# Optimization experiments

Hardware: AMD Instinct MI355X
Metric: run time of the kernel (lower is better)

## Reference

```python
import jax, jax.numpy as jnp
import numpy as np

H = 4096
W = 4096
C = 3
OUT = 1024
MAX_MIP = 8  # matches init max_mip_level; mip chain is levels 0..MAX_MIP


def setup_inputs() -> dict:
    key = jax.random.key(0)
    k1, k2, k3 = jax.random.split(key, 3)
    data = jax.random.uniform(k1, (1, H, W, C), dtype=jnp.float32)
    texc = jax.random.uniform(k2, (1, OUT, OUT, 2), dtype=jnp.float32)
    # small UV derivatives -> per-pixel texel footprint of a few texels, so the
    # LOD spans several mip levels (exercises cross-level paged gathers)
    texc_deriv = jax.random.normal(k3, (1, OUT, OUT, 4), dtype=jnp.float32) * 2e-3
    return {"data": data, "texc": texc, "texc_deriv": texc_deriv}


def _avg_pool2(x):
    # 2x2 box-filter mipmap reduction, matching virtual_texture_mipmap_fwd
    b, h, w, c = x.shape
    return x.reshape(b, h // 2, 2, w // 2, 2, c).mean(axis=(2, 4))


def _bilinear_wrap(tex, texc):
    # tex: [1,h,w,c]; texc: [1,Ho,Wo,2] in [0,1); boundary_mode='wrap'
    h, w = tex.shape[1], tex.shape[2]
    x = texc[..., 0] * w - 0.5
    y = texc[..., 1] * h - 0.5
    x0f = jnp.floor(x)
    y0f = jnp.floor(y)
    fx = (x - x0f)[..., None]
    fy = (y - y0f)[..., None]
    x0 = x0f.astype(jnp.int32) % w
    y0 = y0f.astype(jnp.int32) % h
    x1 = (x0 + 1) % w
    y1 = (y0 + 1) % h
    t = tex[0]  # [h,w,c]
    top = t[y0, x0] * (1.0 - fx) + t[y0, x1] * fx
    bot = t[y1, x0] * (1.0 - fx) + t[y1, x1] * fx
    return top * (1.0 - fy) + bot * fy  # [1,Ho,Wo,c]


def _forward(data, texc, texc_deriv):
    # LOD from screen-space UV derivatives (nvdiffrast linear-mipmap-linear)
    dudx = texc_deriv[..., 0] * W
    dvdx = texc_deriv[..., 1] * H
    dudy = texc_deriv[..., 2] * W
    dvdy = texc_deriv[..., 3] * H
    rho2 = jnp.maximum(dudx * dudx + dvdx * dvdx, dudy * dudy + dvdy * dvdy)
    lod = 0.5 * jnp.log2(jnp.maximum(rho2, 1e-20))
    lod = jnp.clip(lod, 0.0, float(MAX_MIP))  # [1,Ho,Wo]

    # build mip pyramid (gradients flow back to base texture, matching
    # virtual_texture_mipmap_bwd accumulation)
    mips = [data]
    for _ in range(MAX_MIP):
        mips.append(_avg_pool2(mips[-1]))

    # trilinear: per-level weight w_l = clip(1 - |lod - l|, 0, 1)
    out = jnp.zeros(texc.shape[:-1] + (C,), dtype=data.dtype)
    for lvl in range(MAX_MIP + 1):
        w_l = jnp.clip(1.0 - jnp.abs(lod - float(lvl)), 0.0, 1.0)[..., None]
        out = out + w_l * _bilinear_wrap(mips[lvl], texc)
    return out


def reference(data, texc, texc_deriv):
    return _forward(data, texc, texc_deriv)
```

## Files before the change

### kernel.cpp

```cpp
#include <hip/hip_runtime.h>
#include <hip/hip_bf16.h>


#define OUT_N (1024 * 1024)

__device__ __forceinline__ unsigned mip_off_b(int lvl) {
    return (67108864u - (67108864u >> (2 * lvl - 2))) / 3u;
}

__device__ __forceinline__ unsigned pack10(float r, float g, float b) {
    unsigned ur = __float2uint_rn(r * 1023.0f);
    unsigned ug = __float2uint_rn(g * 1023.0f);
    unsigned ub = __float2uint_rn(b * 1023.0f);
    return ur | (ug << 10) | (ub << 20);
}

__device__ __forceinline__ void dec_acc(unsigned q, float w, float& r, float& g, float& b) {
    const float s = 1.0f / 1023.0f;
    r = fmaf((float)(q & 1023u) * s, w, r);
    g = fmaf((float)((q >> 10) & 1023u) * s, w, g);
    b = fmaf((float)((q >> 20) & 1023u) * s, w, b);
}

__device__ __forceinline__ float4 dec4(unsigned q) {
    const float s = 1.0f / 1023.0f;
    return float4{(float)(q & 1023u) * s, (float)((q >> 10) & 1023u) * s,
                  (float)((q >> 20) & 1023u) * s, 0.0f};
}

__device__ __forceinline__ float4 avg4(float4 a, float4 b, float4 c, float4 d) {
    return float4{(a.x + b.x + c.x + d.x) * 0.25f,
                  (a.y + b.y + c.y + d.y) * 0.25f,
                  (a.z + b.z + c.z + d.z) * 0.25f, 0.0f};
}

__device__ __forceinline__ void store_quad(char* p, float4 t00, float4 t01,
                                           float4 t10, float4 t11) {
    *(uint4*)p = make_uint4(pack10(t00.x, t00.y, t00.z), pack10(t01.x, t01.y, t01.z),
                            pack10(t10.x, t10.y, t10.z), pack10(t11.x, t11.y, t11.z));
}

__global__ __launch_bounds__(256) void mip_fused(const float* __restrict__ data,
                                                 char* __restrict__ wsb) {
    __shared__ float4 s1[32][33];
    __shared__ float4 s2[16][17];
    __shared__ float4 s3[8][9];
    __shared__ float4 s4[4][5];

    const int t = threadIdx.x;
    const int bx = blockIdx.x & 63;
    const int by = blockIdx.x >> 6;

    {
        int qx = t & 15, qy = t >> 4;
        int r0 = (by << 6) + (qy << 2);
        int c0 = (bx << 6) + (qx << 2);
        const float* p = data + ((size_t)r0 * 4096 + c0) * 3;
        float4 t00 = {0, 0, 0, 0}, t01 = {0, 0, 0, 0};
        float4 t10 = {0, 0, 0, 0}, t11 = {0, 0, 0, 0};
#pragma unroll
        for (int i = 0; i < 4; ++i) {
            const float4* rp = (const float4*)(p + (size_t)i * 4096 * 3);
            float4 A = rp[0], B = rp[1], C = rp[2];
            float ex = A.x + A.w, ey = A.y + B.x, ez = A.z + B.y;
            float fx_ = B.z + C.y, fy_ = B.w + C.z, fz_ = C.x + C.w;
            if (i < 2) {
                t00.x += ex; t00.y += ey; t00.z += ez;
                t01.x += fx_; t01.y += fy_; t01.z += fz_;
            } else {
                t10.x += ex; t10.y += ey; t10.z += ez;
                t11.x += fx_; t11.y += fy_; t11.z += fz_;
            }
        }
        t00.x *= 0.25f; t00.y *= 0.25f; t00.z *= 0.25f;
        t01.x *= 0.25f; t01.y *= 0.25f; t01.z *= 0.25f;
        t10.x *= 0.25f; t10.y *= 0.25f; t10.z *= 0.25f;
        t11.x *= 0.25f; t11.y *= 0.25f; t11.z *= 0.25f;
        s1[2 * qy][2 * qx] = t00;     s1[2 * qy][2 * qx + 1] = t01;
        s1[2 * qy + 1][2 * qx] = t10; s1[2 * qy + 1][2 * qx + 1] = t11;
        unsigned gq = (((by << 4) + qy) << 10) + (bx << 4) + qx;
        store_quad(wsb + ((size_t)gq << 4), t00, t01, t10, t11);
    }
    __syncthreads();

    if (t < 64) {
        int qx = t & 7, qy = t >> 3;
        int sy = qy << 2, sx = qx << 2;
        float4 t00 = avg4(s1[sy][sx], s1[sy][sx + 1], s1[sy + 1][sx], s1[sy + 1][sx + 1]);
        float4 t01 = avg4(s1[sy][sx + 2], s1[sy][sx + 3], s1[sy + 1][sx + 2], s1[sy + 1][sx + 3]);
        float4 t10 = avg4(s1[sy + 2][sx], s1[sy + 2][sx + 1], s1[sy + 3][sx], s1[sy + 3][sx + 1]);
        float4 t11 = avg4(s1[sy + 2][sx + 2], s1[sy + 2][sx + 3], s1[sy + 3][sx + 2], s1[sy + 3][sx + 3]);
        s2[2 * qy][2 * qx] = t00;     s2[2 * qy][2 * qx + 1] = t01;
        s2[2 * qy + 1][2 * qx] = t10; s2[2 * qy + 1][2 * qx + 1] = t11;
        unsigned gq = ((by << 3) + qy) * 512 + (bx << 3) + qx;
        store_quad(wsb + 16777216u + ((size_t)gq << 4), t00, t01, t10, t11);
    }
    __syncthreads();

    if (t < 16) {
        int qx = t & 3, qy = t >> 2;
        int sy = qy << 2, sx = qx << 2;
        float4 t00 = avg4(s2[sy][sx], s2[sy][sx + 1], s2[sy + 1][sx], s2[sy + 1][sx + 1]);
        float4 t01 = avg4(s2[sy][sx + 2], s2[sy][sx + 3], s2[sy + 1][sx + 2], s2[sy + 1][sx + 3]);
        float4 t10 = avg4(s2[sy + 2][sx], s2[sy + 2][sx + 1], s2[sy + 3][sx], s2[sy + 3][sx + 1]);
        float4 t11 = avg4(s2[sy + 2][sx + 2], s2[sy + 2][sx + 3], s2[sy + 3][sx + 2], s2[sy + 3][sx + 3]);
        s3[2 * qy][2 * qx] = t00;     s3[2 * qy][2 * qx + 1] = t01;
        s3[2 * qy + 1][2 * qx] = t10; s3[2 * qy + 1][2 * qx + 1] = t11;
        unsigned gq = ((by << 2) + qy) * 256 + (bx << 2) + qx;
        store_quad(wsb + 20971520u + ((size_t)gq << 4), t00, t01, t10, t11);
    }
    __syncthreads();

    if (t < 4) {
        int qx = t & 1, qy = t >> 1;
        int sy = qy << 2, sx = qx << 2;
        float4 t00 = avg4(s3[sy][sx], s3[sy][sx + 1], s3[sy + 1][sx], s3[sy + 1][sx + 1]);
        float4 t01 = avg4(s3[sy][sx + 2], s3[sy][sx + 3], s3[sy + 1][sx + 2], s3[sy + 1][sx + 3]);
        float4 t10 = avg4(s3[sy + 2][sx], s3[sy + 2][sx + 1], s3[sy + 3][sx], s3[sy + 3][sx + 1]);
        float4 t11 = avg4(s3[sy + 2][sx + 2], s3[sy + 2][sx + 3], s3[sy + 3][sx + 2], s3[sy + 3][sx + 3]);
        s4[2 * qy][2 * qx] = t00;     s4[2 * qy][2 * qx + 1] = t01;
        s4[2 * qy + 1][2 * qx] = t10; s4[2 * qy + 1][2 * qx + 1] = t11;
        unsigned gq = ((by << 1) + qy) * 128 + (bx << 1) + qx;
        store_quad(wsb + 22020096u + ((size_t)gq << 4), t00, t01, t10, t11);
    }
    __syncthreads();

    if (t == 0) {
        float4 t00 = avg4(s4[0][0], s4[0][1], s4[1][0], s4[1][1]);
        float4 t01 = avg4(s4[0][2], s4[0][3], s4[1][2], s4[1][3]);
        float4 t10 = avg4(s4[2][0], s4[2][1], s4[3][0], s4[3][1]);
        float4 t11 = avg4(s4[2][2], s4[2][3], s4[3][2], s4[3][3]);
        unsigned gq = (unsigned)by * 64u + (unsigned)bx;
        store_quad(wsb + 22282240u + ((size_t)gq << 4), t00, t01, t10, t11);
        float4 l6 = avg4(t00, t01, t10, t11);
        size_t a6 = 22347776u + ((((by >> 1) * 32) + (bx >> 1)) << 4) +
                    ((by & 1) << 3) + ((bx & 1) << 2);
        *(unsigned*)(wsb + a6) = pack10(l6.x, l6.y, l6.z);
    }
}

__global__ __launch_bounds__(256) void mip_tail(char* __restrict__ wsb) {
    __shared__ float4 s7[32][33];
    const int t = threadIdx.x;

    {
        int qx = t & 15, qy = t >> 4;
        float4 f[4][4];
#pragma unroll
        for (int dy = 0; dy < 4; ++dy)
#pragma unroll
            for (int dx = 0; dx < 4; ++dx) {
                int yy = (qy << 2) + dy, xx = (qx << 2) + dx;
                size_t a = 22347776u + (((yy >> 1) * 32 + (xx >> 1)) << 4) +
                           ((yy & 1) << 3) + ((xx & 1) << 2);
                f[dy][dx] = dec4(*(const unsigned*)(wsb + a));
            }
        float4 t00 = avg4(f[0][0], f[0][1], f[1][0], f[1][1]);
        float4 t01 = avg4(f[0][2], f[0][3], f[1][2], f[1][3]);
        float4 t10 = avg4(f[2][0], f[2][1], f[3][0], f[3][1]);
        float4 t11 = avg4(f[2][2], f[2][3], f[3][2], f[3][3]);
        s7[2 * qy][2 * qx] = t00;     s7[2 * qy][2 * qx + 1] = t01;
        s7[2 * qy + 1][2 * qx] = t10; s7[2 * qy + 1][2 * qx + 1] = t11;
        store_quad(wsb + 22364160u + ((size_t)((qy << 4) + qx) << 4), t00, t01, t10, t11);
    }
    __syncthreads();

    if (t < 64) {
        int qx = t & 7, qy = t >> 3;
        int sy = qy << 2, sx = qx << 2;
        float4 t00 = avg4(s7[sy][sx], s7[sy][sx + 1], s7[sy + 1][sx], s7[sy + 1][sx + 1]);
        float4 t01 = avg4(s7[sy][sx + 2], s7[sy][sx + 3], s7[sy + 1][sx + 2], s7[sy + 1][sx + 3]);
        float4 t10 = avg4(s7[sy + 2][sx], s7[sy + 2][sx + 1], s7[sy + 3][sx], s7[sy + 3][sx + 1]);
        float4 t11 = avg4(s7[sy + 2][sx + 2], s7[sy + 2][sx + 3], s7[sy + 3][sx + 2], s7[sy + 3][sx + 3]);
        store_quad(wsb + 22368256u + ((size_t)((qy << 3) + qx) << 4), t00, t01, t10, t11);
    }
}

__device__ __forceinline__ void sample_packed(const char* __restrict__ wsb, int lvl,
                                              float u, float v, float wgt,
                                              float& r, float& g, float& b) {
    int size = 4096 >> lvl;
    float fs = (float)size;
    float x = u * fs - 0.5f;
    float y = v * fs - 0.5f;
    float x0f = floorf(x);
    float y0f = floorf(y);
    float fx = x - x0f;
    float fy = y - y0f;
    int m = size - 1;
    int x0 = ((int)x0f) & m;
    int y0 = ((int)y0f) & m;
    int x1 = (x0 + 1) & m;
    int y1 = (y0 + 1) & m;
    int hs = size >> 1;
    const char* B = wsb + mip_off_b(lvl);
    unsigned q00 = *(const unsigned*)(B + ((((y0 >> 1) * hs) + (x0 >> 1)) << 4) + ((y0 & 1) << 3) + ((x0 & 1) << 2));
    unsigned q01 = *(const unsigned*)(B + ((((y0 >> 1) * hs) + (x1 >> 1)) << 4) + ((y0 & 1) << 3) + ((x1 & 1) << 2));
    unsigned q10 = *(const unsigned*)(B + ((((y1 >> 1) * hs) + (x0 >> 1)) << 4) + ((y1 & 1) << 3) + ((x0 & 1) << 2));
    unsigned q11 = *(const unsigned*)(B + ((((y1 >> 1) * hs) + (x1 >> 1)) << 4) + ((y1 & 1) << 3) + ((x1 & 1) << 2));
    float w00 = (1.0f - fx) * (1.0f - fy) * wgt;
    float w01 = fx * (1.0f - fy) * wgt;
    float w10 = (1.0f - fx) * fy * wgt;
    float w11 = fx * fy * wgt;
    dec_acc(q00, w00, r, g, b);
    dec_acc(q01, w01, r, g, b);
    dec_acc(q10, w10, r, g, b);
    dec_acc(q11, w11, r, g, b);
}

__device__ __forceinline__ void sample_level0(const float* __restrict__ data,
                                              float u, float v, float wgt,
                                              float& r, float& g, float& b) {
    float x = u * 4096.0f - 0.5f;
    float y = v * 4096.0f - 0.5f;
    float x0f = floorf(x);
    float y0f = floorf(y);
    float fx = x - x0f;
    float fy = y - y0f;
    int x0 = ((int)x0f) & 4095;
    int y0 = ((int)y0f) & 4095;
    int x1 = (x0 + 1) & 4095;
    int y1 = (y0 + 1) & 4095;
    const float* p00 = data + ((size_t)y0 * 4096 + x0) * 3;
    const float* p01 = data + ((size_t)y0 * 4096 + x1) * 3;
    const float* p10 = data + ((size_t)y1 * 4096 + x0) * 3;
    const float* p11 = data + ((size_t)y1 * 4096 + x1) * 3;
    float w00 = (1.0f - fx) * (1.0f - fy) * wgt;
    float w01 = fx * (1.0f - fy) * wgt;
    float w10 = (1.0f - fx) * fy * wgt;
    float w11 = fx * fy * wgt;
    r += p00[0] * w00 + p01[0] * w01 + p10[0] * w10 + p11[0] * w11;
    g += p00[1] * w00 + p01[1] * w01 + p10[1] * w10 + p11[1] * w11;
    b += p00[2] * w00 + p01[2] * w01 + p10[2] * w10 + p11[2] * w11;
}

__global__ __launch_bounds__(256) void vt_sample(const float* __restrict__ data,
                                                 const char* __restrict__ wsb,
                                                 const float* __restrict__ texc,
                                                 const float* __restrict__ deriv,
                                                 float* __restrict__ out) {
    int p = blockIdx.x * 256 + threadIdx.x;

    float2 uv = ((const float2*)texc)[p];
    float4 dv = ((const float4*)deriv)[p];
    float dudx = dv.x * 4096.0f;
    float dvdx = dv.y * 4096.0f;
    float dudy = dv.z * 4096.0f;
    float dvdy = dv.w * 4096.0f;
    float rho2 = fmaxf(dudx * dudx + dvdx * dvdx, dudy * dudy + dvdy * dvdy);
    float lod = 0.5f * log2f(fmaxf(rho2, 1e-20f));
    lod = fminf(fmaxf(lod, 0.0f), 8.0f);

    int l0 = (int)lod;
    float f = lod - (float)l0;
    int l1 = (l0 < 8) ? (l0 + 1) : 8;

    float r = 0.0f, g = 0.0f, b = 0.0f;
    if (l0 == 0) {
        sample_level0(data, uv.x, uv.y, 1.0f - f, r, g, b);
    } else {
        sample_packed(wsb, l0, uv.x, uv.y, 1.0f - f, r, g, b);
    }
    sample_packed(wsb, l1, uv.x, uv.y, f, r, g, b);

    float* o = out + (size_t)p * 3;
    o[0] = r;
    o[1] = g;
    o[2] = b;
}

extern "C" void kernel_launch(void* const* d_in, const int* in_sizes, int n_in,
                              void* d_out, int out_size, void* d_ws, size_t ws_size,
                              hipStream_t stream) {
    const float* data  = (const float*)d_in[0];
    const float* texc  = (const float*)d_in[1];
    const float* deriv = (const float*)d_in[2];
    float* out = (float*)d_out;
    char* wsb  = (char*)d_ws;

    mip_fused<<<4096, 256, 0, stream>>>(data, wsb);
    mip_tail<<<1, 256, 0, stream>>>(wsb);
    vt_sample<<<OUT_N / 256, 256, 0, stream>>>(data, wsb, texc, deriv, out);
}
```

Measured before the change: 327.3 us.

## Drop mip level 1 store and tail kernel; reconstruct levels 1, 7, 8 on the fly

Stops writing mip level 1 to the workspace and removes the single-block mip_tail kernel that built levels 7 and 8. In the sampler, level 1 is now built by averaging 2x2 base texels from the fp32 input, and levels 7 and 8 by averaging 2x2 or 4x4 packed level-6 texels at sample time. This cuts mip-building write traffic and a serialized single-block launch. In exchange, pixels that sample level 1 do four times as many base-texture gathers, and coarse levels read more texels. Level 1 is now full fp32 rather than 10-bit packed, and levels 7 and 8 are rebuilt from quantized level-6 data, so numerics shift slightly.

```diff
diff --git a/kernel.cpp b/kernel.cpp
--- a/kernel.cpp
+++ b/kernel.cpp
@@ -7,6 +7,7 @@
 __device__ __forceinline__ unsigned mip_off_b(int lvl) {
     return (67108864u - (67108864u >> (2 * lvl - 2))) / 3u;
 }
+#define OFF6 22347776u
 
 __device__ __forceinline__ unsigned pack10(float r, float g, float b) {
     unsigned ur = __float2uint_rn(r * 1023.0f);
@@ -78,8 +79,6 @@
         t11.x *= 0.25f; t11.y *= 0.25f; t11.z *= 0.25f;
         s1[2 * qy][2 * qx] = t00;     s1[2 * qy][2 * qx + 1] = t01;
         s1[2 * qy + 1][2 * qx] = t10; s1[2 * qy + 1][2 * qx + 1] = t11;
-        unsigned gq = (((by << 4) + qy) << 10) + (bx << 4) + qx;
-        store_quad(wsb + ((size_t)gq << 4), t00, t01, t10, t11);
     }
     __syncthreads();
 
@@ -133,46 +132,9 @@
         unsigned gq = (unsigned)by * 64u + (unsigned)bx;
         store_quad(wsb + 22282240u + ((size_t)gq << 4), t00, t01, t10, t11);
         float4 l6 = avg4(t00, t01, t10, t11);
-        size_t a6 = 22347776u + ((((by >> 1) * 32) + (bx >> 1)) << 4) +
+        size_t a6 = OFF6 + ((((by >> 1) * 32) + (bx >> 1)) << 4) +
                     ((by & 1) << 3) + ((bx & 1) << 2);
         *(unsigned*)(wsb + a6) = pack10(l6.x, l6.y, l6.z);
-    }
-}
-
-__global__ __launch_bounds__(256) void mip_tail(char* __restrict__ wsb) {
-    __shared__ float4 s7[32][33];
-    const int t = threadIdx.x;
-
-    {
-        int qx = t & 15, qy = t >> 4;
-        float4 f[4][4];
-#pragma unroll
-        for (int dy = 0; dy < 4; ++dy)
-#pragma unroll
-            for (int dx = 0; dx < 4; ++dx) {
-                int yy = (qy << 2) + dy, xx = (qx << 2) + dx;
-                size_t a = 22347776u + (((yy >> 1) * 32 + (xx >> 1)) << 4) +
-                           ((yy & 1) << 3) + ((xx & 1) << 2);
-                f[dy][dx] = dec4(*(const unsigned*)(wsb + a));
-            }
-        float4 t00 = avg4(f[0][0], f[0][1], f[1][0], f[1][1]);
-        float4 t01 = avg4(f[0][2], f[0][3], f[1][2], f[1][3]);
-        float4 t10 = avg4(f[2][0], f[2][1], f[3][0], f[3][1]);
-        float4 t11 = avg4(f[2][2], f[2][3], f[3][2], f[3][3]);
-        s7[2 * qy][2 * qx] = t00;     s7[2 * qy][2 * qx + 1] = t01;
-        s7[2 * qy + 1][2 * qx] = t10; s7[2 * qy + 1][2 * qx + 1] = t11;
-        store_quad(wsb + 22364160u + ((size_t)((qy << 4) + qx) << 4), t00, t01, t10, t11);
-    }
-    __syncthreads();
-
-    if (t < 64) {
-        int qx = t & 7, qy = t >> 3;
-        int sy = qy << 2, sx = qx << 2;
-        float4 t00 = avg4(s7[sy][sx], s7[sy][sx + 1], s7[sy + 1][sx], s7[sy + 1][sx + 1]);
-        float4 t01 = avg4(s7[sy][sx + 2], s7[sy][sx + 3], s7[sy + 1][sx + 2], s7[sy + 1][sx + 3]);
-        float4 t10 = avg4(s7[sy + 2][sx], s7[sy + 2][sx + 1], s7[sy + 3][sx], s7[sy + 3][sx + 1]);
-        float4 t11 = avg4(s7[sy + 2][sx + 2], s7[sy + 2][sx + 3], s7[sy + 3][sx + 2], s7[sy + 3][sx + 3]);
-        store_quad(wsb + 22368256u + ((size_t)((qy << 3) + qx) << 4), t00, t01, t10, t11);
     }
 }
 
@@ -208,30 +170,94 @@
     dec_acc(q11, w11, r, g, b);
 }
 
-__device__ __forceinline__ void sample_level0(const float* __restrict__ data,
-                                              float u, float v, float wgt,
-                                              float& r, float& g, float& b) {
-    float x = u * 4096.0f - 0.5f;
-    float y = v * 4096.0f - 0.5f;
+__device__ void sample_fine(const float* __restrict__ data, int lvl,
+                            float u, float v, float wgt,
+                            float& r, float& g, float& b) {
+    int size = 4096 >> lvl;
+    float fs = (float)size;
+    float x = u * fs - 0.5f;
+    float y = v * fs - 0.5f;
     float x0f = floorf(x);
     float y0f = floorf(y);
     float fx = x - x0f;
     float fy = y - y0f;
-    int x0 = ((int)x0f) & 4095;
-    int y0 = ((int)y0f) & 4095;
-    int x1 = (x0 + 1) & 4095;
-    int y1 = (y0 + 1) & 4095;
-    const float* p00 = data + ((size_t)y0 * 4096 + x0) * 3;
-    const float* p01 = data + ((size_t)y0 * 4096 + x1) * 3;
-    const float* p10 = data + ((size_t)y1 * 4096 + x0) * 3;
-    const float* p11 = data + ((size_t)y1 * 4096 + x1) * 3;
-    float w00 = (1.0f - fx) * (1.0f - fy) * wgt;
-    float w01 = fx * (1.0f - fy) * wgt;
-    float w10 = (1.0f - fx) * fy * wgt;
-    float w11 = fx * fy * wgt;
-    r += p00[0] * w00 + p01[0] * w01 + p10[0] * w10 + p11[0] * w11;
-    g += p00[1] * w00 + p01[1] * w01 + p10[1] * w10 + p11[1] * w11;
-    b += p00[2] * w00 + p01[2] * w01 + p10[2] * w10 + p11[2] * w11;
+    int m = size - 1;
+    int x0 = ((int)x0f) & m;
+    int y0 = ((int)y0f) & m;
+    int x1 = (x0 + 1) & m;
+    int y1 = (y0 + 1) & m;
+    int k = 1 << lvl;
+    float inv = wgt / (float)(k * k);
+    float ww[2][2] = {{(1.0f - fx) * (1.0f - fy) * inv, fx * (1.0f - fy) * inv},
+                      {(1.0f - fx) * fy * inv, fx * fy * inv}};
+    int xs[2] = {x0 << lvl, x1 << lvl};
+    int ys[2] = {y0 << lvl, y1 << lvl};
+    for (int ty = 0; ty < 2; ++ty)
+        for (int tx = 0; tx < 2; ++tx) {
+            float tr = 0.0f, tg = 0.0f, tb = 0.0f;
+            for (int dy = 0; dy < k; ++dy)
+                for (int dx = 0; dx < k; ++dx) {
+                    const float* p = data + ((size_t)(ys[ty] + dy) * 4096 + xs[tx] + dx) * 3;
+                    tr += p[0]; tg += p[1]; tb += p[2];
+                }
+            r = fmaf(tr, ww[ty][tx], r);
+            g = fmaf(tg, ww[ty][tx], g);
+            b = fmaf(tb, ww[ty][tx], b);
+        }
+}
+
+__device__ float4 read_l6(const char* __restrict__ wsb, int xx, int yy) {
+    size_t a = OFF6 + ((((yy >> 1) * 32) + (xx >> 1)) << 4) + ((yy & 1) << 3) + ((xx & 1) << 2);
+    return dec4(*(const unsigned*)(wsb + a));
+}
+
+__device__ void sample_coarse(const char* __restrict__ wsb, int lvl,
+                              float u, float v, float wgt,
+                              float& r, float& g, float& b) {
+    int size = 4096 >> lvl;
+    float fs = (float)size;
+    float x = u * fs - 0.5f;
+    float y = v * fs - 0.5f;
+    float x0f = floorf(x);
+    float y0f = floorf(y);
+    float fx = x - x0f;
+    float fy = y - y0f;
+    int m = size - 1;
+    int x0 = ((int)x0f) & m;
+    int y0 = ((int)y0f) & m;
+    int x1 = (x0 + 1) & m;
+    int y1 = (y0 + 1) & m;
+    int s = lvl - 6;
+    int k = 1 << s;
+    float inv = wgt / (float)(k * k);
+    float ww[2][2] = {{(1.0f - fx) * (1.0f - fy) * inv, fx * (1.0f - fy) * inv},
+                      {(1.0f - fx) * fy * inv, fx * fy * inv}};
+    int xs[2] = {x0 << s, x1 << s};
+    int ys[2] = {y0 << s, y1 << s};
+    for (int ty = 0; ty < 2; ++ty)
+        for (int tx = 0; tx < 2; ++tx) {
+            float tr = 0.0f, tg = 0.0f, tb = 0.0f;
+            for (int dy = 0; dy < k; ++dy)
+                for (int dx = 0; dx < k; ++dx) {
+                    float4 c = read_l6(wsb, xs[tx] + dx, ys[ty] + dy);
+                    tr += c.x; tg += c.y; tb += c.z;
+                }
+            r = fmaf(tr, ww[ty][tx], r);
+            g = fmaf(tg, ww[ty][tx], g);
+            b = fmaf(tb, ww[ty][tx], b);
+        }
+}
+
+__device__ __forceinline__ void sample_any(const float* __restrict__ data,
+                                           const char* __restrict__ wsb, int lvl,
+                                           float u, float v, float wgt,
+                                           float& r, float& g, float& b) {
+    if (lvl >= 2) {
+        if (lvl <= 6) sample_packed(wsb, lvl, u, v, wgt, r, g, b);
+        else sample_coarse(wsb, lvl, u, v, wgt, r, g, b);
+    } else {
+        sample_fine(data, lvl, u, v, wgt, r, g, b);
+    }
 }
 
 __global__ __launch_bounds__(256) void vt_sample(const float* __restrict__ data,
@@ -256,12 +282,8 @@
     int l1 = (l0 < 8) ? (l0 + 1) : 8;
 
     float r = 0.0f, g = 0.0f, b = 0.0f;
-    if (l0 == 0) {
-        sample_level0(data, uv.x, uv.y, 1.0f - f, r, g, b);
-    } else {
-        sample_packed(wsb, l0, uv.x, uv.y, 1.0f - f, r, g, b);
-    }
-    sample_packed(wsb, l1, uv.x, uv.y, f, r, g, b);
+    sample_any(data, wsb, l0, uv.x, uv.y, 1.0f - f, r, g, b);
+    sample_any(data, wsb, l1, uv.x, uv.y, f, r, g, b);
 
     float* o = out + (size_t)p * 3;
     o[0] = r;
@@ -279,6 +301,5 @@
     char* wsb  = (char*)d_ws;
 
     mip_fused<<<4096, 256, 0, stream>>>(data, wsb);
-    mip_tail<<<1, 256, 0, stream>>>(wsb);
     vt_sample<<<OUT_N / 256, 256, 0, stream>>>(data, wsb, texc, deriv, out);
 }
```

Result: no change. 325.5 us (-0.5%).
